# Optimization experiments

Measured on AMD Instinct MI355X. Metric: run time of the kernel, lower is better.

The kernel has to match this reference:

```python
import jax, jax.numpy as jnp
import numpy as np
from jax import lax

KH, KW = 3, 3
CIN, F = 32, 32
WSIZE = KH * KW * CIN * F  # 9216


def setup_inputs() -> dict:
    key = jax.random.key(0)
    k1, k2 = jax.random.split(key)
    x = jax.random.normal(k1, (32, 128, 128, CIN), dtype=jnp.float32)
    # hypernetwork output: per-sample flattened kernel (+ bias)
    params = jax.random.normal(k2, (32, WSIZE + F), dtype=jnp.float32) * 0.05
    return {"x": x, "params": params}


def reference(x, params):
    B = x.shape[0]
    # kernel_shape = (kh, kw, input_dim, filters) per keras channels_last
    W = params[:, :WSIZE].reshape(B, KH, KW, CIN, F)  # [B, kh, kw, Cin, F]
    b = params[:, WSIZE:]                              # [B, F]

    def conv_one(xi, wi, bi):
        # xi: [H, W, Cin], wi: [kh, kw, Cin, F] (HWIO), bi: [F]
        out = lax.conv_general_dilated(
            xi[None], wi,
            window_strides=(1, 1), padding="SAME",
            dimension_numbers=("NHWC", "HWIO", "NHWC"),
        )
        return out[0] + bi  # broadcast bias over H, W

    # per-sample dynamic convolution, vectorized over batch
    return jax.vmap(conv_one)(x, W, b)  # activation=None -> linear
```

## Files before the change

kernel.cpp:

```cpp
#include <hip/hip_runtime.h>


typedef __attribute__((ext_vector_type(8))) short bf16x8;
typedef __attribute__((ext_vector_type(4))) float f32x4;

constexpr int HWD  = 128, CINC = 32, FC = 32;
constexpr int WSZ  = 9 * CINC * FC;
constexpr int PSTR = WSZ + FC;

constexpr int XS_PLANE  = 4 * 130 * 16;
constexpr int XS_BYTES  = 4 * (XS_PLANE + 32);
constexpr int WT_BYTES  = 36 * 32 * 16;

constexpr size_t WS_FRAGS = 32ull * 36 * 32;
constexpr size_t WS_NEED  = WS_FRAGS * 16;

__device__ __forceinline__ int xs_off(int cig, int r, int col) {
    return ((cig * 4 + r) * 130 + col) * 16 + cig * 32;
}
__device__ __forceinline__ int wt_off(int kgrp, int f) {
    return XS_BYTES + (kgrp * 32 + f) * 16;
}

__device__ __forceinline__ unsigned short f2bf(float f) {
    unsigned u = __float_as_uint(f);
    return (unsigned short)((u + 0x7FFFu + ((u >> 16) & 1u)) >> 16);
}
__device__ __forceinline__ bf16x8 pack8(float4 a, float4 b) {
    bf16x8 r;
    r[0] = (short)f2bf(a.x); r[1] = (short)f2bf(a.y);
    r[2] = (short)f2bf(a.z); r[3] = (short)f2bf(a.w);
    r[4] = (short)f2bf(b.x); r[5] = (short)f2bf(b.y);
    r[6] = (short)f2bf(b.z); r[7] = (short)f2bf(b.w);
    return r;
}

__device__ __forceinline__ unsigned pk2(float lo, float hi) {
    const unsigned a = __float_as_uint(lo) + 0x8000u;
    const unsigned b = __float_as_uint(hi) + 0x8000u;
    return __builtin_amdgcn_perm(b, a, 0x07060302u);
}
__device__ __forceinline__ bf16x8 pack8f(float4 a, float4 b) {
    union { int4 i; bf16x8 h; } u;
    u.i.x = (int)pk2(a.x, a.y);
    u.i.y = (int)pk2(a.z, a.w);
    u.i.z = (int)pk2(b.x, b.y);
    u.i.w = (int)pk2(b.z, b.w);
    return u.h;
}

__global__ __launch_bounds__(256) void wprep(
    const float* __restrict__ params, bf16x8* __restrict__ ws)
{
    const int b   = blockIdx.y;
    const int seg = blockIdx.x;
    const float* __restrict__ pw = params + (size_t)b * PSTR;
    #pragma unroll
    for (int i = 0; i < 2; ++i) {
        const int idx = threadIdx.x + i * 256;
        if (idx < 288) {
            const int c  = seg * 288 + idx;
            const int sg = c >> 5;
            const int f  = c & 31;
            const float* p = pw + (size_t)(sg * 8) * FC + f;
            float4 a, bb;
            a.x  = p[0 * FC]; a.y  = p[1 * FC]; a.z  = p[2 * FC]; a.w  = p[3 * FC];
            bb.x = p[4 * FC]; bb.y = p[5 * FC]; bb.z = p[6 * FC]; bb.w = p[7 * FC];
            ws[(size_t)b * 1152 + c] = pack8(a, bb);
        }
    }
}

template<bool USE_WS>
__global__ __launch_bounds__(256, USE_WS ? 4 : 3) void conv3x3_mfma(
    const float* __restrict__ x, const float* __restrict__ params,
    float* __restrict__ out, const bf16x8* __restrict__ ws)
{
    __shared__ __align__(16) unsigned char smem[XS_BYTES + (USE_WS ? 0 : WT_BYTES)];

    const int hw      = blockIdx.x;
    const int logical = (hw & 7) * 256 + (hw >> 3);
    const int b       = logical >> 6;
    const int y0      = (logical & 63) * 2;

    const int t = threadIdx.x;
    const float* __restrict__ xb = x + (size_t)b * (HWD * HWD * CINC);
    const float* __restrict__ pw = params + (size_t)b * PSTR;

    const int wv   = t >> 6;
    const int ln   = t & 63;
    const int lg   = ln >> 4;
    const int li   = ln & 15;
    const int yloc = wv >> 1;
    const int xw   = (wv & 1) * 64;

    const size_t wsb = (size_t)b * 1152 + lg * 32;

    float4 xr[9][2];
    bool   inr[9];
    #pragma unroll
    for (int i = 0; i < 9; ++i) {
        const int c = t + i * 256;
        const int cig      = c & 3;
        const unsigned q   = (unsigned)(c >> 2);
        const unsigned r   = q / 130u;
        const unsigned col = q - r * 130u;
        const int iy   = y0 - 1 + (int)r;
        const int icol = (int)col - 1;
        inr[i] = (c < 2080) && ((unsigned)iy < 128u) && ((unsigned)icol < 128u);
        if (inr[i]) {
            const float* p = xb + ((size_t)iy * HWD + icol) * CINC + cig * 8;
            xr[i][0] = *(const float4*)(p);
            xr[i][1] = *(const float4*)(p + 4);
        }
    }

    bf16x8 bc0, bc1;
    if constexpr (USE_WS) {
        bc0 = ws[wsb + li];
        bc1 = ws[wsb + 16 + li];
    }

    #pragma unroll
    for (int i = 0; i < 9; ++i) {
        const int c = t + i * 256;
        if (c < 2080) {
            const int cig      = c & 3;
            const unsigned q   = (unsigned)(c >> 2);
            const unsigned r   = q / 130u;
            const unsigned col = q - r * 130u;
            bf16x8 v = 0;
            if (inr[i]) v = pack8f(xr[i][0], xr[i][1]);
            *(bf16x8*)(smem + xs_off(cig, (int)r, (int)col)) = v;
        }
    }

    if constexpr (!USE_WS) {
        #pragma unroll
        for (int j = 0; j < 5; ++j) {
            const int c    = t + j * 256;
            const int kgrp = c >> 5;
            const int f    = c & 31;
            if (kgrp < 36) {
                const float* p = pw + (size_t)(kgrp * 8) * FC + f;
                float4 a, bb;
                a.x  = p[0 * FC]; a.y  = p[1 * FC]; a.z  = p[2 * FC]; a.w  = p[3 * FC];
                bb.x = p[4 * FC]; bb.y = p[5 * FC]; bb.z = p[6 * FC]; bb.w = p[7 * FC];
                *(bf16x8*)(smem + wt_off(kgrp, f)) = pack8(a, bb);
            }
        }
    }
    __syncthreads();

    f32x4 acc[4][2];
    #pragma unroll
    for (int i = 0; i < 4; ++i) { acc[i][0] = (f32x4)0.0f; acc[i][1] = (f32x4)0.0f; }

    #pragma unroll
    for (int s = 0; s < 9; ++s) {
        const int kh = s / 3, kw = s % 3;
        bf16x8 b0, b1, bn0, bn1;
        if constexpr (USE_WS) {
            if (s < 8) {
                bn0 = ws[wsb + (s + 1) * 128 + li];
                bn1 = ws[wsb + (s + 1) * 128 + 16 + li];
            }
            b0 = bc0; b1 = bc1;
        } else {
            b0 = *(const bf16x8*)(smem + wt_off(s * 4 + lg, li));
            b1 = *(const bf16x8*)(smem + wt_off(s * 4 + lg, 16 + li));
        }
        const int r = yloc + kh;
        const int colbase = xw + li + kw;
        #pragma unroll
        for (int tI = 0; tI < 4; ++tI) {
            const bf16x8 a = *(const bf16x8*)(smem + xs_off(lg, r, colbase + tI * 16));
            acc[tI][0] = __builtin_amdgcn_mfma_f32_16x16x32_bf16(b0, a, acc[tI][0], 0, 0, 0);
            acc[tI][1] = __builtin_amdgcn_mfma_f32_16x16x32_bf16(b1, a, acc[tI][1], 0, 0, 0);
        }
        if constexpr (USE_WS) { bc0 = bn0; bc1 = bn1; }
    }

    const float4 bias0 = *(const float4*)(pw + WSZ + lg * 4);
    const float4 bias1 = *(const float4*)(pw + WSZ + 16 + lg * 4);
    const int yo = y0 + yloc;
    float* __restrict__ ob = out + ((size_t)(b * HWD + yo)) * (HWD * FC);

    #pragma unroll
    for (int tI = 0; tI < 4; ++tI) {
        const int px = xw + tI * 16 + li;
        float* q = ob + (size_t)px * FC + lg * 4;
        float4 v0, v1;
        v0.x = acc[tI][0][0] + bias0.x; v0.y = acc[tI][0][1] + bias0.y;
        v0.z = acc[tI][0][2] + bias0.z; v0.w = acc[tI][0][3] + bias0.w;
        v1.x = acc[tI][1][0] + bias1.x; v1.y = acc[tI][1][1] + bias1.y;
        v1.z = acc[tI][1][2] + bias1.z; v1.w = acc[tI][1][3] + bias1.w;
        *(float4*)(q)      = v0;
        *(float4*)(q + 16) = v1;
    }
}

extern "C" void kernel_launch(void* const* d_in, const int* in_sizes, int n_in,
                              void* d_out, int out_size, void* d_ws, size_t ws_size,
                              hipStream_t stream)
{
    const float* x      = (const float*)d_in[0];
    const float* params = (const float*)d_in[1];
    float*       out    = (float*)d_out;

    if (ws_size >= WS_NEED && d_ws != nullptr) {
        bf16x8* ws = (bf16x8*)d_ws;
        hipLaunchKernelGGL(wprep, dim3(4, 32), dim3(256), 0, stream, params, ws);
        hipLaunchKernelGGL((conv3x3_mfma<true>), dim3(2048), dim3(256), 0, stream,
                           x, params, out, (const bf16x8*)ws);
    } else {
        hipLaunchKernelGGL((conv3x3_mfma<false>), dim3(2048), dim3(256), 0, stream,
                           x, params, out, (const bf16x8*)nullptr);
    }
}
```

Before: 130.4 us.

## Make conv blocks persistent over four row pairs with double-buffered LDS prefetch

Each block now handles four 2-row output tiles instead of one, cutting the grid from 2048 to 512 blocks. Input rows for the next tile are loaded into registers while the current tile runs its MFMAs, using two LDS buffers. This aims to hide global-load latency and reduce per-block setup. In exchange it doubles LDS use, lowers the occupancy hint to 2, and leaves only 512 blocks on a 256-CU device, which risks poor load balance.

```diff
diff --git a/kernel.cpp b/kernel.cpp
--- a/kernel.cpp
+++ b/kernel.cpp
@@ -19,7 +19,7 @@
     return ((cig * 4 + r) * 130 + col) * 16 + cig * 32;
 }
 __device__ __forceinline__ int wt_off(int kgrp, int f) {
-    return XS_BYTES + (kgrp * 32 + f) * 16;
+    return 2 * XS_BYTES + (kgrp * 32 + f) * 16;
 }
 
 __device__ __forceinline__ unsigned short f2bf(float f) {
@@ -72,16 +72,16 @@
 }
 
 template<bool USE_WS>
-__global__ __launch_bounds__(256, USE_WS ? 4 : 3) void conv3x3_mfma(
+__global__ __launch_bounds__(256, 2) void conv3x3_mfma(
     const float* __restrict__ x, const float* __restrict__ params,
     float* __restrict__ out, const bf16x8* __restrict__ ws)
 {
-    __shared__ __align__(16) unsigned char smem[XS_BYTES + (USE_WS ? 0 : WT_BYTES)];
-
-    const int hw      = blockIdx.x;
-    const int logical = (hw & 7) * 256 + (hw >> 3);
-    const int b       = logical >> 6;
-    const int y0      = (logical & 63) * 2;
+    __shared__ __align__(16) unsigned char smem[2 * XS_BYTES + (USE_WS ? 0 : WT_BYTES)];
+
+    const int hw  = blockIdx.x;
+    const int swz = (hw & 7) * 64 + (hw >> 3);
+    const int b   = swz >> 4;
+    const int qrp = swz & 15;
 
     const int t = threadIdx.x;
     const float* __restrict__ xb = x + (size_t)b * (HWD * HWD * CINC);
@@ -96,44 +96,37 @@
 
     const size_t wsb = (size_t)b * 1152 + lg * 32;
 
-    float4 xr[9][2];
-    bool   inr[9];
+    int  r_i[9], ldsoff_i[9], xoff_i[9];
+    bool colok_i[9];
     #pragma unroll
     for (int i = 0; i < 9; ++i) {
         const int c = t + i * 256;
         const int cig      = c & 3;
-        const unsigned q   = (unsigned)(c >> 2);
-        const unsigned r   = q / 130u;
-        const unsigned col = q - r * 130u;
-        const int iy   = y0 - 1 + (int)r;
+        const unsigned q2  = (unsigned)(c >> 2);
+        const unsigned r   = q2 / 130u;
+        const unsigned col = q2 - r * 130u;
         const int icol = (int)col - 1;
-        inr[i] = (c < 2080) && ((unsigned)iy < 128u) && ((unsigned)icol < 128u);
-        if (inr[i]) {
-            const float* p = xb + ((size_t)iy * HWD + icol) * CINC + cig * 8;
-            xr[i][0] = *(const float4*)(p);
-            xr[i][1] = *(const float4*)(p + 4);
-        }
-    }
-
-    bf16x8 bc0, bc1;
-    if constexpr (USE_WS) {
-        bc0 = ws[wsb + li];
-        bc1 = ws[wsb + 16 + li];
-    }
-
-    #pragma unroll
-    for (int i = 0; i < 9; ++i) {
-        const int c = t + i * 256;
-        if (c < 2080) {
-            const int cig      = c & 3;
-            const unsigned q   = (unsigned)(c >> 2);
-            const unsigned r   = q / 130u;
-            const unsigned col = q - r * 130u;
-            bf16x8 v = 0;
-            if (inr[i]) v = pack8f(xr[i][0], xr[i][1]);
-            *(bf16x8*)(smem + xs_off(cig, (int)r, (int)col)) = v;
-        }
-    }
+        r_i[i]      = (int)r;
+        colok_i[i]  = (c < 2080) && ((unsigned)icol < 128u);
+        ldsoff_i[i] = xs_off(cig, (int)r, (int)col);
+        xoff_i[i]   = icol * CINC + cig * 8;
+    }
+
+    float4 xr[9][2];
+    bool   inr[9];
+
+    auto stage_issue = [&](int y0t) {
+        #pragma unroll
+        for (int i = 0; i < 9; ++i) {
+            const int iy = y0t - 1 + r_i[i];
+            inr[i] = colok_i[i] && ((unsigned)iy < 128u);
+            if (inr[i]) {
+                const float* p = xb + (size_t)iy * (HWD * CINC) + xoff_i[i];
+                xr[i][0] = *(const float4*)(p);
+                xr[i][1] = *(const float4*)(p + 4);
+            }
+        }
+    };
 
     if constexpr (!USE_WS) {
         #pragma unroll
@@ -150,53 +143,76 @@
             }
         }
     }
-    __syncthreads();
-
-    f32x4 acc[4][2];
-    #pragma unroll
-    for (int i = 0; i < 4; ++i) { acc[i][0] = (f32x4)0.0f; acc[i][1] = (f32x4)0.0f; }
-
-    #pragma unroll
-    for (int s = 0; s < 9; ++s) {
-        const int kh = s / 3, kw = s % 3;
-        bf16x8 b0, b1, bn0, bn1;
-        if constexpr (USE_WS) {
-            if (s < 8) {
-                bn0 = ws[wsb + (s + 1) * 128 + li];
-                bn1 = ws[wsb + (s + 1) * 128 + 16 + li];
-            }
-            b0 = bc0; b1 = bc1;
-        } else {
-            b0 = *(const bf16x8*)(smem + wt_off(s * 4 + lg, li));
-            b1 = *(const bf16x8*)(smem + wt_off(s * 4 + lg, 16 + li));
-        }
-        const int r = yloc + kh;
-        const int colbase = xw + li + kw;
-        #pragma unroll
-        for (int tI = 0; tI < 4; ++tI) {
-            const bf16x8 a = *(const bf16x8*)(smem + xs_off(lg, r, colbase + tI * 16));
-            acc[tI][0] = __builtin_amdgcn_mfma_f32_16x16x32_bf16(b0, a, acc[tI][0], 0, 0, 0);
-            acc[tI][1] = __builtin_amdgcn_mfma_f32_16x16x32_bf16(b1, a, acc[tI][1], 0, 0, 0);
-        }
-        if constexpr (USE_WS) { bc0 = bn0; bc1 = bn1; }
-    }
 
     const float4 bias0 = *(const float4*)(pw + WSZ + lg * 4);
     const float4 bias1 = *(const float4*)(pw + WSZ + 16 + lg * 4);
-    const int yo = y0 + yloc;
-    float* __restrict__ ob = out + ((size_t)(b * HWD + yo)) * (HWD * FC);
-
-    #pragma unroll
-    for (int tI = 0; tI < 4; ++tI) {
-        const int px = xw + tI * 16 + li;
-        float* q = ob + (size_t)px * FC + lg * 4;
-        float4 v0, v1;
-        v0.x = acc[tI][0][0] + bias0.x; v0.y = acc[tI][0][1] + bias0.y;
-        v0.z = acc[tI][0][2] + bias0.z; v0.w = acc[tI][0][3] + bias0.w;
-        v1.x = acc[tI][1][0] + bias1.x; v1.y = acc[tI][1][1] + bias1.y;
-        v1.z = acc[tI][1][2] + bias1.z; v1.w = acc[tI][1][3] + bias1.w;
-        *(float4*)(q)      = v0;
-        *(float4*)(q + 16) = v1;
+
+    stage_issue(qrp * 2);
+    for (int tt = 0; tt < 4; ++tt) {
+        const int y0t = (qrp + tt * 16) * 2;
+        unsigned char* __restrict__ sb = smem + (tt & 1) * XS_BYTES;
+
+        #pragma unroll
+        for (int i = 0; i < 9; ++i) {
+            if (t + i * 256 < 2080) {
+                bf16x8 v = 0;
+                if (inr[i]) v = pack8f(xr[i][0], xr[i][1]);
+                *(bf16x8*)(sb + ldsoff_i[i]) = v;
+            }
+        }
+        __syncthreads();
+
+        if (tt < 3) stage_issue((qrp + (tt + 1) * 16) * 2);
+
+        f32x4 acc[4][2];
+        #pragma unroll
+        for (int i = 0; i < 4; ++i) { acc[i][0] = (f32x4)0.0f; acc[i][1] = (f32x4)0.0f; }
+
+        bf16x8 bc0, bc1;
+        if constexpr (USE_WS) {
+            bc0 = ws[wsb + li];
+            bc1 = ws[wsb + 16 + li];
+        }
+
+        #pragma unroll
+        for (int s = 0; s < 9; ++s) {
+            const int kh = s / 3, kw = s % 3;
+            bf16x8 b0, b1, bn0, bn1;
+            if constexpr (USE_WS) {
+                if (s < 8) {
+                    bn0 = ws[wsb + (s + 1) * 128 + li];
+                    bn1 = ws[wsb + (s + 1) * 128 + 16 + li];
+                }
+                b0 = bc0; b1 = bc1;
+            } else {
+                b0 = *(const bf16x8*)(smem + wt_off(s * 4 + lg, li));
+                b1 = *(const bf16x8*)(smem + wt_off(s * 4 + lg, 16 + li));
+            }
+            const int r = yloc + kh;
+            const int colbase = xw + li + kw;
+            #pragma unroll
+            for (int tI = 0; tI < 4; ++tI) {
+                const bf16x8 a = *(const bf16x8*)(sb + xs_off(lg, r, colbase + tI * 16));
+                acc[tI][0] = __builtin_amdgcn_mfma_f32_16x16x32_bf16(b0, a, acc[tI][0], 0, 0, 0);
+                acc[tI][1] = __builtin_amdgcn_mfma_f32_16x16x32_bf16(b1, a, acc[tI][1], 0, 0, 0);
+            }
+            if constexpr (USE_WS) { bc0 = bn0; bc1 = bn1; }
+        }
+
+        const int yo = y0t + yloc;
+        float* __restrict__ ob = out + ((size_t)(b * HWD + yo)) * (HWD * FC);
+        #pragma unroll
+        for (int tI = 0; tI < 4; ++tI) {
+            const int px = xw + tI * 16 + li;
+            float* q = ob + (size_t)px * FC + lg * 4;
+            float4 v0, v1;
+            v0.x = acc[tI][0][0] + bias0.x; v0.y = acc[tI][0][1] + bias0.y;
+            v0.z = acc[tI][0][2] + bias0.z; v0.w = acc[tI][0][3] + bias0.w;
+            v1.x = acc[tI][1][0] + bias1.x; v1.y = acc[tI][1][1] + bias1.y;
+            v1.z = acc[tI][1][2] + bias1.z; v1.w = acc[tI][1][3] + bias1.w;
+            *(float4*)(q)      = v0;
+            *(float4*)(q + 16) = v1;
+        }
     }
 }
 
@@ -211,10 +227,10 @@
     if (ws_size >= WS_NEED && d_ws != nullptr) {
         bf16x8* ws = (bf16x8*)d_ws;
         hipLaunchKernelGGL(wprep, dim3(4, 32), dim3(256), 0, stream, params, ws);
-        hipLaunchKernelGGL((conv3x3_mfma<true>), dim3(2048), dim3(256), 0, stream,
+        hipLaunchKernelGGL((conv3x3_mfma<true>), dim3(512), dim3(256), 0, stream,
                            x, params, out, (const bf16x8*)ws);
     } else {
-        hipLaunchKernelGGL((conv3x3_mfma<false>), dim3(2048), dim3(256), 0, stream,
+        hipLaunchKernelGGL((conv3x3_mfma<false>), dim3(512), dim3(256), 0, stream,
                            x, params, out, (const bf16x8*)nullptr);
     }
 }
```

New measurement: 130.3 us. About the same (-0.1%).

## Stream fp32 input rows into LDS via async DMA with persistent 16-row bands

Applied to the files above, without the earlier changes.

Restructures the conv kernel so each block handles a 64-column by 16-row band. For each group of 4 output rows it stages 6 input rows of raw fp32 into a swizzled LDS layout with global_load_lds DMA, zero-fills halo chunks afterwards, and converts to bf16 at fragment read time with v_cvt_pk_bf16_f32. The grid shrinks from 2048 to 512 blocks, and the next stage's loads are issued before the output stores to overlap them. This reduces the number of halo rows loaded per output row and removes the register round-trip conversion. In exchange it uses more LDS, lowers occupancy to 2 blocks, has a serial vmcnt(0) wait per stage, and does extra conversion work on every MFMA operand.

```diff
diff --git a/kernel.cpp b/kernel.cpp
--- a/kernel.cpp
+++ b/kernel.cpp
@@ -3,24 +3,17 @@
 
 typedef __attribute__((ext_vector_type(8))) short bf16x8;
 typedef __attribute__((ext_vector_type(4))) float f32x4;
+typedef __attribute__((ext_vector_type(4))) int   i32x4;
 
 constexpr int HWD  = 128, CINC = 32, FC = 32;
 constexpr int WSZ  = 9 * CINC * FC;
 constexpr int PSTR = WSZ + FC;
 
-constexpr int XS_PLANE  = 4 * 130 * 16;
-constexpr int XS_BYTES  = 4 * (XS_PLANE + 32);
-constexpr int WT_BYTES  = 36 * 32 * 16;
-
-constexpr size_t WS_FRAGS = 32ull * 36 * 32;
-constexpr size_t WS_NEED  = WS_FRAGS * 16;
-
-__device__ __forceinline__ int xs_off(int cig, int r, int col) {
-    return ((cig * 4 + r) * 130 + col) * 16 + cig * 32;
-}
-__device__ __forceinline__ int wt_off(int kgrp, int f) {
-    return XS_BYTES + (kgrp * 32 + f) * 16;
-}
+constexpr int ROW_CHUNKS = 528;
+constexpr int ROW_BYTES  = 576 * 16;
+constexpr int LDS_BYTES  = 6 * ROW_BYTES;
+
+constexpr size_t WS_NEED = 32ull * 36 * 32 * 16;
 
 __device__ __forceinline__ unsigned short f2bf(float f) {
     unsigned u = __float_as_uint(f);
@@ -35,18 +28,19 @@
     return r;
 }
 
-__device__ __forceinline__ unsigned pk2(float lo, float hi) {
-    const unsigned a = __float_as_uint(lo) + 0x8000u;
-    const unsigned b = __float_as_uint(hi) + 0x8000u;
-    return __builtin_amdgcn_perm(b, a, 0x07060302u);
-}
-__device__ __forceinline__ bf16x8 pack8f(float4 a, float4 b) {
-    union { int4 i; bf16x8 h; } u;
-    u.i.x = (int)pk2(a.x, a.y);
-    u.i.y = (int)pk2(a.z, a.w);
-    u.i.z = (int)pk2(b.x, b.y);
-    u.i.w = (int)pk2(b.z, b.w);
+__device__ __forceinline__ bf16x8 cvtpk8(float4 lo, float4 hi) {
+    union { i32x4 i; bf16x8 h; } u;
+    asm("v_cvt_pk_bf16_f32 %0, %1, %2" : "=v"(u.i.x) : "v"(lo.x), "v"(lo.y));
+    asm("v_cvt_pk_bf16_f32 %0, %1, %2" : "=v"(u.i.y) : "v"(lo.z), "v"(lo.w));
+    asm("v_cvt_pk_bf16_f32 %0, %1, %2" : "=v"(u.i.z) : "v"(hi.x), "v"(hi.y));
+    asm("v_cvt_pk_bf16_f32 %0, %1, %2" : "=v"(u.i.w) : "v"(hi.z), "v"(hi.w));
     return u.h;
+}
+
+__device__ __forceinline__ void dma16(const void* src, void* lds_dst) {
+    __builtin_amdgcn_global_load_lds(
+        (const __attribute__((address_space(1))) unsigned int*)src,
+        (__attribute__((address_space(3))) unsigned int*)lds_dst, 16, 0, 0);
 }
 
 __global__ __launch_bounds__(256) void wprep(
@@ -72,131 +66,147 @@
 }
 
 template<bool USE_WS>
-__global__ __launch_bounds__(256, USE_WS ? 4 : 3) void conv3x3_mfma(
+__global__ __launch_bounds__(256, 2) void conv3x3_mfma(
     const float* __restrict__ x, const float* __restrict__ params,
     float* __restrict__ out, const bf16x8* __restrict__ ws)
 {
-    __shared__ __align__(16) unsigned char smem[XS_BYTES + (USE_WS ? 0 : WT_BYTES)];
-
-    const int hw      = blockIdx.x;
-    const int logical = (hw & 7) * 256 + (hw >> 3);
-    const int b       = logical >> 6;
-    const int y0      = (logical & 63) * 2;
-
-    const int t = threadIdx.x;
+    __shared__ __align__(16) unsigned char smem[LDS_BYTES];
+
+    const int hw   = blockIdx.x;
+    const int swz  = (hw & 7) * 64 + (hw >> 3);
+    const int b    = swz >> 4;
+    const int half = (swz >> 3) & 1;
+    const int band = swz & 7;
+    const int X0   = half * 64;
+    const int R0   = band * 16;
+
+    const int t  = threadIdx.x;
+    const int wv = t >> 6;
+    const int ln = t & 63;
+    const int lg = ln >> 4;
+    const int li = ln & 15;
+
     const float* __restrict__ xb = x + (size_t)b * (HWD * HWD * CINC);
     const float* __restrict__ pw = params + (size_t)b * PSTR;
-
-    const int wv   = t >> 6;
-    const int ln   = t & 63;
-    const int lg   = ln >> 4;
-    const int li   = ln & 15;
-    const int yloc = wv >> 1;
-    const int xw   = (wv & 1) * 64;
-
     const size_t wsb = (size_t)b * 1152 + lg * 32;
-
-    float4 xr[9][2];
-    bool   inr[9];
-    #pragma unroll
-    for (int i = 0; i < 9; ++i) {
-        const int c = t + i * 256;
-        const int cig      = c & 3;
-        const unsigned q   = (unsigned)(c >> 2);
-        const unsigned r   = q / 130u;
-        const unsigned col = q - r * 130u;
-        const int iy   = y0 - 1 + (int)r;
-        const int icol = (int)col - 1;
-        inr[i] = (c < 2080) && ((unsigned)iy < 128u) && ((unsigned)icol < 128u);
-        if (inr[i]) {
-            const float* p = xb + ((size_t)iy * HWD + icol) * CINC + cig * 8;
-            xr[i][0] = *(const float4*)(p);
-            xr[i][1] = *(const float4*)(p + 4);
-        }
-    }
-
-    bf16x8 bc0, bc1;
-    if constexpr (USE_WS) {
-        bc0 = ws[wsb + li];
-        bc1 = ws[wsb + 16 + li];
-    }
-
-    #pragma unroll
-    for (int i = 0; i < 9; ++i) {
-        const int c = t + i * 256;
-        if (c < 2080) {
-            const int cig      = c & 3;
-            const unsigned q   = (unsigned)(c >> 2);
-            const unsigned r   = q / 130u;
-            const unsigned col = q - r * 130u;
-            bf16x8 v = 0;
-            if (inr[i]) v = pack8f(xr[i][0], xr[i][1]);
-            *(bf16x8*)(smem + xs_off(cig, (int)r, (int)col)) = v;
-        }
-    }
-
-    if constexpr (!USE_WS) {
-        #pragma unroll
-        for (int j = 0; j < 5; ++j) {
-            const int c    = t + j * 256;
-            const int kgrp = c >> 5;
-            const int f    = c & 31;
-            if (kgrp < 36) {
-                const float* p = pw + (size_t)(kgrp * 8) * FC + f;
-                float4 a, bb;
-                a.x  = p[0 * FC]; a.y  = p[1 * FC]; a.z  = p[2 * FC]; a.w  = p[3 * FC];
-                bb.x = p[4 * FC]; bb.y = p[5 * FC]; bb.z = p[6 * FC]; bb.w = p[7 * FC];
-                *(bf16x8*)(smem + wt_off(kgrp, f)) = pack8(a, bb);
-            }
-        }
-    }
-    __syncthreads();
-
-    f32x4 acc[4][2];
-    #pragma unroll
-    for (int i = 0; i < 4; ++i) { acc[i][0] = (f32x4)0.0f; acc[i][1] = (f32x4)0.0f; }
-
-    #pragma unroll
-    for (int s = 0; s < 9; ++s) {
-        const int kh = s / 3, kw = s % 3;
-        bf16x8 b0, b1, bn0, bn1;
-        if constexpr (USE_WS) {
-            if (s < 8) {
-                bn0 = ws[wsb + (s + 1) * 128 + li];
-                bn1 = ws[wsb + (s + 1) * 128 + 16 + li];
-            }
-            b0 = bc0; b1 = bc1;
-        } else {
-            b0 = *(const bf16x8*)(smem + wt_off(s * 4 + lg, li));
-            b1 = *(const bf16x8*)(smem + wt_off(s * 4 + lg, 16 + li));
-        }
-        const int r = yloc + kh;
-        const int colbase = xw + li + kw;
-        #pragma unroll
-        for (int tI = 0; tI < 4; ++tI) {
-            const bf16x8 a = *(const bf16x8*)(smem + xs_off(lg, r, colbase + tI * 16));
-            acc[tI][0] = __builtin_amdgcn_mfma_f32_16x16x32_bf16(b0, a, acc[tI][0], 0, 0, 0);
-            acc[tI][1] = __builtin_amdgcn_mfma_f32_16x16x32_bf16(b1, a, acc[tI][1], 0, 0, 0);
-        }
-        if constexpr (USE_WS) { bc0 = bn0; bc1 = bn1; }
-    }
 
     const float4 bias0 = *(const float4*)(pw + WSZ + lg * 4);
     const float4 bias1 = *(const float4*)(pw + WSZ + 16 + lg * 4);
-    const int yo = y0 + yloc;
-    float* __restrict__ ob = out + ((size_t)(b * HWD + yo)) * (HWD * FC);
-
-    #pragma unroll
-    for (int tI = 0; tI < 4; ++tI) {
-        const int px = xw + tI * 16 + li;
-        float* q = ob + (size_t)px * FC + lg * 4;
-        float4 v0, v1;
-        v0.x = acc[tI][0][0] + bias0.x; v0.y = acc[tI][0][1] + bias0.y;
-        v0.z = acc[tI][0][2] + bias0.z; v0.w = acc[tI][0][3] + bias0.w;
-        v1.x = acc[tI][1][0] + bias1.x; v1.y = acc[tI][1][1] + bias1.y;
-        v1.z = acc[tI][1][2] + bias1.z; v1.w = acc[tI][1][3] + bias1.w;
-        *(float4*)(q)      = v0;
-        *(float4*)(q + 16) = v1;
+
+    auto stage = [&](int y0t) {
+        #pragma unroll
+        for (int j = 0; j < 14; ++j) {
+            const int d = wv + j * 4;
+            if (d < 54) {
+                const int rr  = d / 9;
+                const int seg = d - rr * 9;
+                const int s   = seg * 64 + ln;
+                if (s < ROW_CHUNKS) {
+                    const int col = s >> 3;
+                    const int k   = (s & 7) ^ (col & 7);
+                    const int iy  = y0t - 1 + rr;
+                    const int gx  = X0 - 1 + col;
+                    const bool ok = ((unsigned)iy < 128u) && ((unsigned)gx < 128u);
+                    const float* src = ok ? (xb + ((size_t)iy * HWD + gx) * CINC + k * 4)
+                                          : xb;
+                    dma16(src, smem + rr * ROW_BYTES + seg * 1024);
+                }
+            }
+        }
+    };
+    auto fixz = [&](int y0t) {
+        #pragma unroll
+        for (int j = 0; j < 14; ++j) {
+            const int d = wv + j * 4;
+            if (d < 54) {
+                const int rr  = d / 9;
+                const int seg = d - rr * 9;
+                const int s   = seg * 64 + ln;
+                if (s < ROW_CHUNKS) {
+                    const int col = s >> 3;
+                    const int iy  = y0t - 1 + rr;
+                    const int gx  = X0 - 1 + col;
+                    if (!(((unsigned)iy < 128u) && ((unsigned)gx < 128u))) {
+                        i32x4 z = {0, 0, 0, 0};
+                        *(i32x4*)(smem + rr * ROW_BYTES + s * 16) = z;
+                    }
+                }
+            }
+        }
+    };
+
+    stage(R0);
+    asm volatile("s_waitcnt vmcnt(0)" ::: "memory");
+    fixz(R0);
+    __syncthreads();
+
+    for (int tt = 0; tt < 4; ++tt) {
+        const int y0t = R0 + tt * 4;
+
+        f32x4 acc[4][2];
+        #pragma unroll
+        for (int i = 0; i < 4; ++i) { acc[i][0] = (f32x4)0.0f; acc[i][1] = (f32x4)0.0f; }
+
+        bf16x8 bc0, bc1;
+        if constexpr (USE_WS) { bc0 = ws[wsb + li]; bc1 = ws[wsb + 16 + li]; }
+
+        #pragma unroll
+        for (int s9 = 0; s9 < 9; ++s9) {
+            const int kh = s9 / 3, kw = s9 - 3 * (s9 / 3);
+            bf16x8 b0, b1, bn0, bn1;
+            if constexpr (USE_WS) {
+                if (s9 < 8) {
+                    bn0 = ws[wsb + (s9 + 1) * 128 + li];
+                    bn1 = ws[wsb + (s9 + 1) * 128 + 16 + li];
+                }
+                b0 = bc0; b1 = bc1;
+            } else {
+                float w0[8], w1[8];
+                #pragma unroll
+                for (int kk = 0; kk < 8; ++kk) {
+                    w0[kk] = pw[(size_t)(s9 * 32 + lg * 8 + kk) * FC + li];
+                    w1[kk] = pw[(size_t)(s9 * 32 + lg * 8 + kk) * FC + 16 + li];
+                }
+                float4 a0{w0[0], w0[1], w0[2], w0[3]}, a1{w0[4], w0[5], w0[6], w0[7]};
+                float4 c0{w1[0], w1[1], w1[2], w1[3]}, c1{w1[4], w1[5], w1[6], w1[7]};
+                b0 = cvtpk8(a0, a1); b1 = cvtpk8(c0, c1);
+            }
+            const unsigned char* rowp = smem + (wv + kh) * ROW_BYTES;
+            #pragma unroll
+            for (int tI = 0; tI < 4; ++tI) {
+                const int col = tI * 16 + li + kw;
+                const int q0  = (2 * lg) ^ (col & 7);
+                const float4 lo = *(const float4*)(rowp + col * 128 + q0 * 16);
+                const float4 hi = *(const float4*)(rowp + col * 128 + (q0 ^ 1) * 16);
+                const bf16x8 a  = cvtpk8(lo, hi);
+                acc[tI][0] = __builtin_amdgcn_mfma_f32_16x16x32_bf16(b0, a, acc[tI][0], 0, 0, 0);
+                acc[tI][1] = __builtin_amdgcn_mfma_f32_16x16x32_bf16(b1, a, acc[tI][1], 0, 0, 0);
+            }
+            if constexpr (USE_WS) { bc0 = bn0; bc1 = bn1; }
+        }
+
+        __syncthreads();
+        if (tt < 3) stage(y0t + 4);
+
+        const int R = y0t + wv;
+        float* __restrict__ ob = out + ((size_t)(b * HWD + R) * HWD + X0) * FC;
+        #pragma unroll
+        for (int tI = 0; tI < 4; ++tI) {
+            float* q = ob + (size_t)(tI * 16 + li) * FC + lg * 4;
+            float4 v0, v1;
+            v0.x = acc[tI][0][0] + bias0.x; v0.y = acc[tI][0][1] + bias0.y;
+            v0.z = acc[tI][0][2] + bias0.z; v0.w = acc[tI][0][3] + bias0.w;
+            v1.x = acc[tI][1][0] + bias1.x; v1.y = acc[tI][1][1] + bias1.y;
+            v1.z = acc[tI][1][2] + bias1.z; v1.w = acc[tI][1][3] + bias1.w;
+            *(float4*)(q)      = v0;
+            *(float4*)(q + 16) = v1;
+        }
+
+        if (tt < 3) {
+            asm volatile("s_waitcnt vmcnt(0)" ::: "memory");
+            fixz(y0t + 4);
+            __syncthreads();
+        }
     }
 }
 
@@ -211,10 +221,10 @@
     if (ws_size >= WS_NEED && d_ws != nullptr) {
         bf16x8* ws = (bf16x8*)d_ws;
         hipLaunchKernelGGL(wprep, dim3(4, 32), dim3(256), 0, stream, params, ws);
-        hipLaunchKernelGGL((conv3x3_mfma<true>), dim3(2048), dim3(256), 0, stream,
+        hipLaunchKernelGGL((conv3x3_mfma<true>), dim3(512), dim3(256), 0, stream,
                            x, params, out, (const bf16x8*)ws);
     } else {
-        hipLaunchKernelGGL((conv3x3_mfma<false>), dim3(2048), dim3(256), 0, stream,
+        hipLaunchKernelGGL((conv3x3_mfma<false>), dim3(512), dim3(256), 0, stream,
                            x, params, out, (const bf16x8*)nullptr);
     }
 }
```

After: 130.9 us. About the same (+0.4%).
